# Optimization experiments

Hardware: AMD Instinct MI355X
Metric: run time of the kernel (lower is better)

Reference implementation:

```python
import jax, jax.numpy as jnp
import numpy as np

B, S, D, H = 4, 1024, 1024, 16
DH = D // H  # head dim = 64
PAD = -1e7   # padding_num in source
EPS = 1e-3   # keras LayerNormalization default epsilon


def setup_inputs() -> dict:
    key = jax.random.key(0)
    ks = jax.random.split(key, 8)
    return {
        "queries": jax.random.normal(ks[0], (B, S, D), jnp.float32),
        "keys": jax.random.normal(ks[1], (B, S, D), jnp.float32),
        "values": jax.random.normal(ks[2], (B, S, D), jnp.float32),
        "query_masks": jax.random.randint(ks[3], (B, S), 0, 2, jnp.int32),
        "key_masks": jax.random.randint(ks[4], (B, S), 0, 2, jnp.int32),
        "Wq": jax.random.normal(ks[5], (D, D), jnp.float32) * (D ** -0.5),
        "Wk": jax.random.normal(ks[6], (D, D), jnp.float32) * (D ** -0.5),
        "Wv": jax.random.normal(ks[7], (D, D), jnp.float32) * (D ** -0.5),
        "gamma": jnp.ones((D,), jnp.float32),
        "beta": jnp.zeros((D,), jnp.float32),
    }


def reference(queries, keys, values, query_masks, key_masks, Wq, Wk, Wv, gamma, beta):
    # QKV projections (no bias)
    Q = queries @ Wq  # [B,S,D]
    K = keys @ Wk
    V = values @ Wv
    # split heads: tf.split(axis=2)+concat(axis=0) == head-major layout [H,B,S,DH]
    Qh = Q.reshape(B, S, H, DH).transpose(2, 0, 1, 3)
    Kh = K.reshape(B, S, H, DH).transpose(2, 0, 1, 3)
    Vh = V.reshape(B, S, H, DH).transpose(2, 0, 1, 3)
    # scaled scores; note source scales by head_dim ** 0.5 (d_k of split K)
    scores = jnp.einsum("hbqd,hbkd->hbqk", Qh, Kh) / (DH ** 0.5)
    # additive key mask: positions where key_mask==0 get large negative
    scores = jnp.where(key_masks[None, :, None, :] == 0, PAD, scores)
    attn = jax.nn.softmax(scores, axis=-1)
    # multiplicative query mask AFTER softmax (as in source)
    attn = attn * query_masks[None, :, :, None].astype(jnp.float32)
    out = jnp.einsum("hbqk,hbkd->hbqd", attn, Vh)  # [H,B,S,DH]
    # merge heads back: concat over feature axis in head order
    out = out.transpose(1, 2, 0, 3).reshape(B, S, D)
    # residual + LayerNorm
    res = queries + out
    mean = jnp.mean(res, axis=-1, keepdims=True)
    var = jnp.mean(jnp.square(res - mean), axis=-1, keepdims=True)
    return gamma * (res - mean) * jax.lax.rsqrt(var + EPS) + beta
```

## Files before the change

### kernel.cpp

```cpp
#include <hip/hip_runtime.h>

#define BB   4
#define SS   1024
#define DD   1024
#define HH   16
#define DHH  64
#define LN_EPS  (1e-3f)

typedef unsigned short u16;
typedef __attribute__((ext_vector_type(8))) short bf16x8;
typedef __attribute__((ext_vector_type(4))) float f32x4;

__device__ __forceinline__ u16 f2bf(float f) {
    union { float f; unsigned int u; } v; v.f = f;
    return (u16)((v.u + 0x7FFFu + ((v.u >> 16) & 1u)) >> 16);
}

__device__ __forceinline__ void cp16(void* lds, const void* g) {
    __builtin_amdgcn_global_load_lds(
        (const __attribute__((address_space(1))) unsigned int*)g,
        (__attribute__((address_space(3))) unsigned int*)lds, 16, 0, 0);
}

__global__ __launch_bounds__(256) void prep(const float* __restrict__ q,
                                            const float* __restrict__ k,
                                            const float* __restrict__ v,
                                            const float* __restrict__ Wq,
                                            const float* __restrict__ Wk,
                                            const float* __restrict__ Wv,
                                            u16* __restrict__ Abf,
                                            u16* __restrict__ WtA) {
    __shared__ float Ts[64][65];
    const int z = blockIdx.z;
    const int tid = threadIdx.x;
    if (z < 3) {
        const float* src = (z == 0) ? q : (z == 1) ? k : v;
        u16* dst = Abf + (size_t)z * ((size_t)BB * SS * DD);
        const int N8 = BB * SS * DD / 8;
        for (int i = blockIdx.x * 256 + tid; i < N8; i += 256 * 256) {
            const float4 f0 = ((const float4*)src)[i * 2];
            const float4 f1 = ((const float4*)src)[i * 2 + 1];
            union { u16 u[8]; uint4 o; } t;
            t.u[0] = f2bf(f0.x); t.u[1] = f2bf(f0.y);
            t.u[2] = f2bf(f0.z); t.u[3] = f2bf(f0.w);
            t.u[4] = f2bf(f1.x); t.u[5] = f2bf(f1.y);
            t.u[6] = f2bf(f1.z); t.u[7] = f2bf(f1.w);
            ((uint4*)dst)[i] = t.o;
        }
    } else {
        const float* W = (z == 3) ? Wq : (z == 4) ? Wk : Wv;
        u16* Wt = WtA + (size_t)(z - 3) * DD * DD;
        const int k0 = (blockIdx.x >> 4) * 64, n0 = (blockIdx.x & 15) * 64;
        #pragma unroll
        for (int it = 0; it < 4; ++it) {
            const int idx = tid + it * 256;
            const int r = idx >> 4, c4 = (idx & 15) * 4;
            const float4 vv = *(const float4*)&W[(size_t)(k0 + r) * DD + n0 + c4];
            Ts[r][c4 + 0] = vv.x; Ts[r][c4 + 1] = vv.y;
            Ts[r][c4 + 2] = vv.z; Ts[r][c4 + 3] = vv.w;
        }
        __syncthreads();
        const int n = tid >> 2, kc = (tid & 3) * 16;
        #pragma unroll
        for (int p = 0; p < 8; ++p) {
            const unsigned int lo = f2bf(Ts[kc + p * 2 + 0][n]);
            const unsigned int hi = f2bf(Ts[kc + p * 2 + 1][n]);
            *(unsigned int*)&Wt[(size_t)(n0 + n) * DD + k0 + kc + p * 2] = lo | (hi << 16);
        }
    }
}

__global__ __launch_bounds__(256) void gemm_fused(const u16* __restrict__ Abf,
                                                  const u16* __restrict__ WtA,
                                                  u16* __restrict__ Qbf,
                                                  u16* __restrict__ Kbf,
                                                  u16* __restrict__ Vtb) {
    __shared__ u16 As[128 * 64];
    __shared__ u16 Bs[128 * 64];
    const int bid = blockIdx.x;
    const int xcd = bid & 7;
    const int t   = bid >> 3;
    const int z   = t >> 5;
    const int rr  = t & 31;
    const int m0  = (xcd * 4 + (rr & 3)) * 128;
    const int n0  = (rr >> 2) * 128;

    const u16* A = Abf + (size_t)z * BB * SS * DD;
    const u16* B = WtA + (size_t)z * DD * DD;
    const int tid  = threadIdx.x;
    const int wave = tid >> 6, lane = tid & 63;
    const int ln = lane & 15, quad = lane >> 4;
    const int mw = (wave & 1) * 64, nw = (wave >> 1) * 64;

    f32x4 acc[4][4] = {};

    for (int k0 = 0; k0 < DD; k0 += 64) {
        __syncthreads();
        #pragma unroll
        for (int w = 0; w < 4; ++w) {
            const int s = w * 256 + wave * 64 + lane;
            const int r = s >> 3, csrc = (s & 7) ^ (r & 7);
            cp16(&As[(size_t)(w * 256 + wave * 64) * 8],
                 &A[(size_t)(m0 + r) * DD + k0 + csrc * 8]);
            cp16(&Bs[(size_t)(w * 256 + wave * 64) * 8],
                 &B[(size_t)(n0 + r) * DD + k0 + csrc * 8]);
        }
        __syncthreads();

        #pragma unroll
        for (int kk = 0; kk < 2; ++kk) {
            bf16x8 af[4], bfv[4];
            #pragma unroll
            for (int i = 0; i < 4; ++i) {
                const int r = mw + i * 16 + ln;
                af[i] = *(const bf16x8*)&As[((r << 3) + ((kk * 4 + quad) ^ (r & 7))) << 3];
            }
            #pragma unroll
            for (int j = 0; j < 4; ++j) {
                const int r = nw + j * 16 + ln;
                bfv[j] = *(const bf16x8*)&Bs[((r << 3) + ((kk * 4 + quad) ^ (r & 7))) << 3];
            }
            #pragma unroll
            for (int i = 0; i < 4; ++i)
                #pragma unroll
                for (int j = 0; j < 4; ++j)
                    acc[i][j] = __builtin_amdgcn_mfma_f32_16x16x32_bf16(af[i], bfv[j], acc[i][j], 0, 0, 0);
        }
    }

    if (z < 2) {
        u16* C = (z == 0) ? Qbf : Kbf;
        const float scale = (z == 0) ? 0.125f : 1.0f;
        #pragma unroll
        for (int i = 0; i < 4; ++i) {
            const int mbase = m0 + mw + i * 16 + quad * 4;
            const int bb = mbase >> 10, sb = mbase & 1023;
            #pragma unroll
            for (int j = 0; j < 4; ++j) {
                const int n = n0 + nw + j * 16 + ln;
                const int hh = n >> 6, dh = n & 63;
                #pragma unroll
                for (int r = 0; r < 4; ++r)
                    C[(((size_t)bb * HH + hh) * SS + sb + r) * DHH + dh] =
                        f2bf(acc[i][j][r] * scale);
            }
        }
    } else {
        #pragma unroll
        for (int i = 0; i < 4; ++i) {
            const int mbase = m0 + mw + i * 16 + quad * 4;
            const int bb = mbase >> 10, sb = mbase & 1023;
            #pragma unroll
            for (int j = 0; j < 4; ++j) {
                const int n = n0 + nw + j * 16 + ln;
                const int hh = n >> 6, dh = n & 63;
                uint2 pk;
                pk.x = (unsigned int)f2bf(acc[i][j][0]) | ((unsigned int)f2bf(acc[i][j][1]) << 16);
                pk.y = (unsigned int)f2bf(acc[i][j][2]) | ((unsigned int)f2bf(acc[i][j][3]) << 16);
                *(uint2*)&Vtb[(((size_t)bb * HH + hh) * DHH + dh) * SS + sb] = pk;
            }
        }
    }
}

__global__ __launch_bounds__(256) void attn_mfma(const u16* __restrict__ Qg,
                                                 const u16* __restrict__ Kg,
                                                 const u16* __restrict__ Vtg,
                                                 const int* __restrict__ qmask,
                                                 const int* __restrict__ kmask,
                                                 float* __restrict__ O) {
    __shared__ u16 QPs[64 * 68];
    __shared__ u16 Ks[64 * 64];
    __shared__ u16 Vs[64 * 64];

    const int bid  = blockIdx.x;
    const int xcd  = bid & 7;
    const int rest = bid >> 3;
    const int bh   = (rest & 7) * 8 + xcd;
    const int qt   = rest >> 3;
    const int b    = bh >> 4, h = bh & 15;
    const int q0   = qt * 64;
    const int tid  = threadIdx.x;
    const int wave = tid >> 6, lane = tid & 63;
    const int ln = lane & 15, quad = lane >> 4;
    const size_t bhs = (size_t)b * HH + h;

    #pragma unroll
    for (int w = 0; w < 2; ++w) {
        const int s = w * 256 + wave * 64 + lane;
        const int r = s >> 3, csrc = (s & 7) ^ (r & 7);
        cp16(&QPs[(size_t)(w * 256 + wave * 64) * 8],
             &Qg[(bhs * SS + q0 + r) * DHH + csrc * 8]);
    }
    __syncthreads();

    bf16x8 qf[2];
    #pragma unroll
    for (int kk = 0; kk < 2; ++kk) {
        const int r = wave * 16 + ln;
        qf[kk] = *(const bf16x8*)&QPs[((r << 3) + ((kk * 4 + quad) ^ (r & 7))) << 3];
    }

    f32x4 o[4] = {};
    float lsum[4] = {0.f, 0.f, 0.f, 0.f};
    const f32x4 zero = {0.f, 0.f, 0.f, 0.f};

    for (int kt = 0; kt < SS / 64; ++kt) {
        __syncthreads();
        #pragma unroll
        for (int w = 0; w < 2; ++w) {
            const int s = w * 256 + wave * 64 + lane;
            const int r = s >> 3, csrc = (s & 7) ^ (r & 7);
            cp16(&Ks[(size_t)(w * 256 + wave * 64) * 8],
                 &Kg[(bhs * SS + kt * 64 + r) * DHH + csrc * 8]);
            cp16(&Vs[(size_t)(w * 256 + wave * 64) * 8],
                 &Vtg[(bhs * DHH + r) * SS + kt * 64 + csrc * 8]);
        }
        __syncthreads();

        #pragma unroll
        for (int nt = 0; nt < 4; ++nt) {
            const int krow = nt * 16 + ln;
            const bf16x8 k0f = *(const bf16x8*)&Ks[((krow << 3) + ((0 + quad) ^ (krow & 7))) << 3];
            const bf16x8 k1f = *(const bf16x8*)&Ks[((krow << 3) + ((4 + quad) ^ (krow & 7))) << 3];
            f32x4 sacc = __builtin_amdgcn_mfma_f32_16x16x32_bf16(qf[0], k0f, zero, 0, 0, 0);
            sacc = __builtin_amdgcn_mfma_f32_16x16x32_bf16(qf[1], k1f, sacc, 0, 0, 0);
            const int km = kmask[b * SS + kt * 64 + krow];
            #pragma unroll
            for (int r = 0; r < 4; ++r) {
                const float p = km ? __expf(sacc[r]) : 0.0f;
                lsum[r] += p;
                QPs[(wave * 16 + quad * 4 + r) * 68 + nt * 16 + ln] = f2bf(p);
            }
        }

        #pragma unroll
        for (int kk2 = 0; kk2 < 2; ++kk2) {
            const bf16x8 pf = *(const bf16x8*)&QPs[(wave * 16 + ln) * 68 + kk2 * 32 + quad * 8];
            #pragma unroll
            for (int nt2 = 0; nt2 < 4; ++nt2) {
                const int vrow = nt2 * 16 + ln;
                const bf16x8 vf = *(const bf16x8*)&Vs[((vrow << 3) + ((kk2 * 4 + quad) ^ (vrow & 7))) << 3];
                o[nt2] = __builtin_amdgcn_mfma_f32_16x16x32_bf16(pf, vf, o[nt2], 0, 0, 0);
            }
        }
    }

    #pragma unroll
    for (int r = 0; r < 4; ++r) {
        #pragma unroll
        for (int off = 1; off < 16; off <<= 1)
            lsum[r] += __shfl_xor(lsum[r], off);
        const int q = q0 + wave * 16 + quad * 4 + r;
        const float scale = (float)qmask[b * SS + q] / lsum[r];
        #pragma unroll
        for (int nt2 = 0; nt2 < 4; ++nt2)
            O[((size_t)b * SS + q) * DD + h * DHH + nt2 * 16 + ln] = o[nt2][r] * scale;
    }
}

__global__ __launch_bounds__(256) void ln_kernel(const float* __restrict__ Qin,
                                                 const float* __restrict__ attn,
                                                 const float* __restrict__ gamma,
                                                 const float* __restrict__ beta,
                                                 float* __restrict__ out) {
    const int row = blockIdx.x;
    const int tid = threadIdx.x;
    const int wid = tid >> 6, lane = tid & 63;
    __shared__ float sred[4];

    const float4 qv = ((const float4*)Qin)[(size_t)row * 256 + tid];
    const float4 av = ((const float4*)attn)[(size_t)row * 256 + tid];
    float4 v;
    v.x = qv.x + av.x; v.y = qv.y + av.y;
    v.z = qv.z + av.z; v.w = qv.w + av.w;

    float sum = v.x + v.y + v.z + v.w;
    #pragma unroll
    for (int off = 32; off; off >>= 1) sum += __shfl_down(sum, off);
    if (lane == 0) sred[wid] = sum;
    __syncthreads();
    const float mean = (sred[0] + sred[1] + sred[2] + sred[3]) * (1.0f / DD);
    __syncthreads();

    const float dx = v.x - mean, dy = v.y - mean, dz = v.z - mean, dw = v.w - mean;
    float vs = dx * dx + dy * dy + dz * dz + dw * dw;
    #pragma unroll
    for (int off = 32; off; off >>= 1) vs += __shfl_down(vs, off);
    if (lane == 0) sred[wid] = vs;
    __syncthreads();
    const float var = (sred[0] + sred[1] + sred[2] + sred[3]) * (1.0f / DD);
    const float inv = rsqrtf(var + LN_EPS);

    const float4 g = ((const float4*)gamma)[tid];
    const float4 bt = ((const float4*)beta)[tid];
    float4 ov;
    ov.x = g.x * dx * inv + bt.x; ov.y = g.y * dy * inv + bt.y;
    ov.z = g.z * dz * inv + bt.z; ov.w = g.w * dw * inv + bt.w;
    ((float4*)out)[(size_t)row * 256 + tid] = ov;
}

extern "C" void kernel_launch(void* const* d_in, const int* in_sizes, int n_in,
                              void* d_out, int out_size, void* d_ws, size_t ws_size,
                              hipStream_t stream) {
    const float* queries = (const float*)d_in[0];
    const float* keys    = (const float*)d_in[1];
    const float* values  = (const float*)d_in[2];
    const int*   qmask   = (const int*)d_in[3];
    const int*   kmask   = (const int*)d_in[4];
    const float* Wq      = (const float*)d_in[5];
    const float* Wk      = (const float*)d_in[6];
    const float* Wv      = (const float*)d_in[7];
    const float* gamma   = (const float*)d_in[8];
    const float* beta    = (const float*)d_in[9];
    float* out = (float*)d_out;

    const size_t NTOK = (size_t)BB * SS;
    u16* Abf = (u16*)d_ws;
    float* Ob = (float*)d_ws;
    u16* Qbf = Abf + 3 * NTOK * DD;
    u16* Kbf = Qbf + NTOK * DD;
    u16* Vtb = Kbf + NTOK * DD;
    u16* WtA = Vtb + NTOK * DD;

    prep<<<dim3(256, 1, 6), 256, 0, stream>>>(queries, keys, values, Wq, Wk, Wv, Abf, WtA);

    gemm_fused<<<768, 256, 0, stream>>>(Abf, WtA, Qbf, Kbf, Vtb);

    attn_mfma<<<BB * HH * (SS / 64), 256, 0, stream>>>(Qbf, Kbf, Vtb, qmask, kmask, Ob);

    ln_kernel<<<BB * SS, 256, 0, stream>>>(queries, Ob, gamma, beta, out);
}
```

Before: 206.9 us.

## Rewrite QKV GEMM with 256x256 tiles and multi-stage async LDS pipeline

The fused QKV projection GEMM moves from 128x128 tiles with 4 waves and a single-buffered LDS load to 256x256 tiles with 8 waves. K-slices are split into halves and prefetched via a double-buffered global_load_lds pipeline with explicit vmcnt waits, and setprio is raised around the MFMA blocks. The aim is more data reuse per block and to hide global-load latency behind MFMA work. In exchange, only 192 blocks are launched, which may underfill the 256 CUs, and the larger accumulator raises register pressure.

```diff
diff --git a/kernel.cpp b/kernel.cpp
--- a/kernel.cpp
+++ b/kernel.cpp
@@ -70,93 +70,134 @@
     }
 }
 
-__global__ __launch_bounds__(256) void gemm_fused(const u16* __restrict__ Abf,
-                                                  const u16* __restrict__ WtA,
-                                                  u16* __restrict__ Qbf,
-                                                  u16* __restrict__ Kbf,
-                                                  u16* __restrict__ Vtb) {
-    __shared__ u16 As[128 * 64];
-    __shared__ u16 Bs[128 * 64];
+__global__ __launch_bounds__(512, 2) void gemm_fused(const u16* __restrict__ Abf,
+                                                     const u16* __restrict__ WtA,
+                                                     u16* __restrict__ Qbf,
+                                                     u16* __restrict__ Kbf,
+                                                     u16* __restrict__ Vtb) {
+    __shared__ u16 lds[2][2][2][8192];
+
     const int bid = blockIdx.x;
-    const int xcd = bid & 7;
-    const int t   = bid >> 3;
-    const int z   = t >> 5;
-    const int rr  = t & 31;
-    const int m0  = (xcd * 4 + (rr & 3)) * 128;
-    const int n0  = (rr >> 2) * 128;
-
-    const u16* A = Abf + (size_t)z * BB * SS * DD;
-    const u16* B = WtA + (size_t)z * DD * DD;
+    const int swz = (bid & 7) * 24 + (bid >> 3);
+    const int z   = swz >> 6;
+    const int rem = swz & 63;
+    const int m0  = (rem >> 2) * 256;
+    const int n0  = (rem & 3) * 256;
+
+    const u16* A  = Abf + (size_t)z * ((size_t)BB * SS * DD);
+    const u16* Bm = WtA + (size_t)z * (DD * DD);
+
     const int tid  = threadIdx.x;
     const int wave = tid >> 6, lane = tid & 63;
     const int ln = lane & 15, quad = lane >> 4;
-    const int mw = (wave & 1) * 64, nw = (wave >> 1) * 64;
-
-    f32x4 acc[4][4] = {};
-
-    for (int k0 = 0; k0 < DD; k0 += 64) {
-        __syncthreads();
-        #pragma unroll
-        for (int w = 0; w < 4; ++w) {
-            const int s = w * 256 + wave * 64 + lane;
-            const int r = s >> 3, csrc = (s & 7) ^ (r & 7);
-            cp16(&As[(size_t)(w * 256 + wave * 64) * 8],
-                 &A[(size_t)(m0 + r) * DD + k0 + csrc * 8]);
-            cp16(&Bs[(size_t)(w * 256 + wave * 64) * 8],
-                 &B[(size_t)(n0 + r) * DD + k0 + csrc * 8]);
-        }
-        __syncthreads();
-
-        #pragma unroll
-        for (int kk = 0; kk < 2; ++kk) {
-            bf16x8 af[4], bfv[4];
-            #pragma unroll
-            for (int i = 0; i < 4; ++i) {
-                const int r = mw + i * 16 + ln;
-                af[i] = *(const bf16x8*)&As[((r << 3) + ((kk * 4 + quad) ^ (r & 7))) << 3];
-            }
-            #pragma unroll
-            for (int j = 0; j < 4; ++j) {
-                const int r = nw + j * 16 + ln;
-                bfv[j] = *(const bf16x8*)&Bs[((r << 3) + ((kk * 4 + quad) ^ (r & 7))) << 3];
-            }
-            #pragma unroll
-            for (int i = 0; i < 4; ++i)
+    const int wr = wave >> 2, wc = wave & 3;
+
+    int r_[2], c_[2];
+    #pragma unroll
+    for (int rd = 0; rd < 2; ++rd) {
+        const int l = rd * 512 + tid;
+        const int rr = l >> 2, cs = l & 3;
+        r_[rd] = rr;
+        c_[rd] = cs ^ ((rr >> 1) & 3);
+    }
+    const u16* srcA[2] = { A  + (size_t)(m0 + r_[0]) * DD + c_[0] * 8,
+                           A  + (size_t)(m0 + r_[1]) * DD + c_[1] * 8 };
+    const u16* srcB[2] = { Bm + (size_t)(n0 + r_[0]) * DD + c_[0] * 8,
+                           Bm + (size_t)(n0 + r_[1]) * DD + c_[1] * 8 };
+
+    int offA[8], offB[4];
+    #pragma unroll
+    for (int mi = 0; mi < 8; ++mi) {
+        const int r = wr * 128 + mi * 16 + ln;
+        offA[mi] = (r * 4 + (quad ^ ((r >> 1) & 3))) * 8;
+    }
+    #pragma unroll
+    for (int nj = 0; nj < 4; ++nj) {
+        const int r = wc * 64 + nj * 16 + ln;
+        offB[nj] = (r * 4 + (quad ^ ((r >> 1) & 3))) * 8;
+    }
+
+    auto stage = [&](int T, int x) {
+        const int cb = T & 1;
+        const int koff = T * 64 + x * 32;
+        #pragma unroll
+        for (int rd = 0; rd < 2; ++rd) {
+            cp16(&lds[cb][x][0][(rd * 512 + wave * 64) * 8], srcA[rd] + koff);
+            cp16(&lds[cb][x][1][(rd * 512 + wave * 64) * 8], srcB[rd] + koff);
+        }
+    };
+
+    f32x4 acc[8][4] = {};
+
+    stage(0, 0); stage(0, 1); stage(1, 0);
+    asm volatile("s_waitcnt vmcnt(8)" ::: "memory");
+    __builtin_amdgcn_s_barrier();
+
+    #pragma unroll
+    for (int t = 0; t < 16; ++t) {
+        const int c = t & 1;
+        #pragma unroll
+        for (int x = 0; x < 2; ++x) {
+            if (x == 0) { if (t < 15) stage(t + 1, 1); }
+            else        { if (t < 14) stage(t + 2, 0); }
+
+            bf16x8 af[8], bfv[4];
+            const u16* Ar = &lds[c][x][0][0];
+            const u16* Br = &lds[c][x][1][0];
+            #pragma unroll
+            for (int mi = 0; mi < 8; ++mi) af[mi] = *(const bf16x8*)&Ar[offA[mi]];
+            #pragma unroll
+            for (int nj = 0; nj < 4; ++nj) bfv[nj] = *(const bf16x8*)&Br[offB[nj]];
+
+            if (x == 0) {
+                if (t < 15) asm volatile("s_waitcnt vmcnt(8)" ::: "memory");
+                else        asm volatile("s_waitcnt vmcnt(0)" ::: "memory");
+            } else {
+                if (t < 14)       asm volatile("s_waitcnt vmcnt(8)" ::: "memory");
+                else if (t == 14) asm volatile("s_waitcnt vmcnt(4)" ::: "memory");
+            }
+            __builtin_amdgcn_s_barrier();
+
+            __builtin_amdgcn_s_setprio(1);
+            #pragma unroll
+            for (int mi = 0; mi < 8; ++mi)
                 #pragma unroll
-                for (int j = 0; j < 4; ++j)
-                    acc[i][j] = __builtin_amdgcn_mfma_f32_16x16x32_bf16(af[i], bfv[j], acc[i][j], 0, 0, 0);
-        }
-    }
-
+                for (int nj = 0; nj < 4; ++nj)
+                    acc[mi][nj] = __builtin_amdgcn_mfma_f32_16x16x32_bf16(
+                        af[mi], bfv[nj], acc[mi][nj], 0, 0, 0);
+            __builtin_amdgcn_s_setprio(0);
+            __builtin_amdgcn_s_barrier();
+        }
+    }
+
+    const int hh = (n0 >> 6) + wc;
     if (z < 2) {
         u16* C = (z == 0) ? Qbf : Kbf;
         const float scale = (z == 0) ? 0.125f : 1.0f;
         #pragma unroll
-        for (int i = 0; i < 4; ++i) {
-            const int mbase = m0 + mw + i * 16 + quad * 4;
+        for (int mi = 0; mi < 8; ++mi) {
+            const int mbase = m0 + wr * 128 + mi * 16 + quad * 4;
             const int bb = mbase >> 10, sb = mbase & 1023;
             #pragma unroll
-            for (int j = 0; j < 4; ++j) {
-                const int n = n0 + nw + j * 16 + ln;
-                const int hh = n >> 6, dh = n & 63;
+            for (int nj = 0; nj < 4; ++nj) {
+                const int dh = nj * 16 + ln;
                 #pragma unroll
                 for (int r = 0; r < 4; ++r)
                     C[(((size_t)bb * HH + hh) * SS + sb + r) * DHH + dh] =
-                        f2bf(acc[i][j][r] * scale);
+                        f2bf(acc[mi][nj][r] * scale);
             }
         }
     } else {
         #pragma unroll
-        for (int i = 0; i < 4; ++i) {
-            const int mbase = m0 + mw + i * 16 + quad * 4;
+        for (int mi = 0; mi < 8; ++mi) {
+            const int mbase = m0 + wr * 128 + mi * 16 + quad * 4;
             const int bb = mbase >> 10, sb = mbase & 1023;
             #pragma unroll
-            for (int j = 0; j < 4; ++j) {
-                const int n = n0 + nw + j * 16 + ln;
-                const int hh = n >> 6, dh = n & 63;
+            for (int nj = 0; nj < 4; ++nj) {
+                const int dh = nj * 16 + ln;
                 uint2 pk;
-                pk.x = (unsigned int)f2bf(acc[i][j][0]) | ((unsigned int)f2bf(acc[i][j][1]) << 16);
-                pk.y = (unsigned int)f2bf(acc[i][j][2]) | ((unsigned int)f2bf(acc[i][j][3]) << 16);
+                pk.x = (unsigned int)f2bf(acc[mi][nj][0]) | ((unsigned int)f2bf(acc[mi][nj][1]) << 16);
+                pk.y = (unsigned int)f2bf(acc[mi][nj][2]) | ((unsigned int)f2bf(acc[mi][nj][3]) << 16);
                 *(uint2*)&Vtb[(((size_t)bb * HH + hh) * DHH + dh) * SS + sb] = pk;
             }
         }
@@ -325,7 +366,7 @@
 
     prep<<<dim3(256, 1, 6), 256, 0, stream>>>(queries, keys, values, Wq, Wk, Wv, Abf, WtA);
 
-    gemm_fused<<<768, 256, 0, stream>>>(Abf, WtA, Qbf, Kbf, Vtb);
+    gemm_fused<<<192, 512, 0, stream>>>(Abf, WtA, Qbf, Kbf, Vtb);
 
     attn_mfma<<<BB * HH * (SS / 64), 256, 0, stream>>>(Qbf, Kbf, Vtb, qmask, kmask, Ob);
 
```

Measured after the change: 199.2 us. 1.04x faster.
